# Kernel tuning notes

Measured on AMD Instinct MI355X. Metric: run time of the kernel, lower is better.

## Reference

```python
import jax, jax.numpy as jnp
import numpy as np

B, C, H, IN = 128, 1024, 256, 19  # batch, subcarriers, hidden, input dim
P = 2 * H                          # prism input dim (att + rad features)
NL = 8                             # layers in attenuation/radiance nets
UEBS = 2 * 4                       # num_ue_antennas * num_bs_antennas


def _init(key, shape, scale=0.02):
    return (jax.random.normal(key, shape, dtype=jnp.float32) * scale)


def setup_inputs() -> dict:
    key = jax.random.key(0)
    ks = jax.random.split(key, 24)
    return {
        "positions": jax.random.normal(ks[0], (B, 3), dtype=jnp.float32),
        "ue_antennas": jax.random.normal(ks[1], (B, 2), dtype=jnp.float32),
        "bs_antennas": jax.random.normal(ks[2], (B, 4), dtype=jnp.float32),
        "additional_features": jax.random.normal(ks[3], (B, 10), dtype=jnp.float32),
        "att_W1": _init(ks[4], (IN, H)), "att_b1": _init(ks[5], (H,)),
        "att_Wh": _init(ks[6], (NL - 1, H, H)), "att_bh": _init(ks[7], (NL - 1, H)),
        # radiance net: same structure
        "rad_W1": _init(ks[8], (IN, H)), "rad_b1": _init(ks[9], (H,)),
        "rad_Wh": _init(ks[10], (NL - 1, H, H)), "rad_bh": _init(ks[11], (NL - 1, H)),
        # RF prism: per-subcarrier stacked weights
        "prism_W1": _init(ks[12], (C, P, H)), "prism_b1": _init(ks[13], (C, H)),
        "prism_W2": _init(ks[14], (C, H, H)), "prism_b2": _init(ks[15], (C, H)),
        "prism_W3": _init(ks[16], (C, H)), "prism_b3": _init(ks[17], (C,)),
        # mimo head: Linear(1 -> ue*bs)
        "mimo_W": _init(ks[18], (1, UEBS)), "mimo_b": _init(ks[19], (UEBS,)),
    }


def _deep_mlp(x, W1, b1, Wh, bh):
    h = jax.nn.relu(x @ W1 + b1)
    def step(h, wb):
        W, b = wb
        return jax.nn.relu(h @ W + b), None
    h, _ = jax.lax.scan(step, h, (Wh, bh))
    return h


def reference(positions, ue_antennas, bs_antennas, additional_features,
              att_W1, att_b1, att_Wh, att_bh,
              rad_W1, rad_b1, rad_Wh, rad_bh,
              prism_W1, prism_b1, prism_W2, prism_b2, prism_W3, prism_b3,
              mimo_W, mimo_b):
    x = jnp.concatenate([positions, ue_antennas, bs_antennas, additional_features], axis=1)  # [B,19]
    att = _deep_mlp(x, att_W1, att_b1, att_Wh, att_bh)  # [B,H]
    rad = _deep_mlp(x, rad_W1, rad_b1, rad_Wh, rad_bh)  # [B,H]
    feat = jnp.concatenate([att, rad], axis=1)  # [B,2H]
    # batched per-subcarrier 3-layer MLPs (grouped GEMMs)
    h1 = jax.nn.relu(jnp.einsum('bi,cio->bco', feat, prism_W1) + prism_b1)  # [B,C,H]
    h2 = jax.nn.relu(jnp.einsum('bch,cho->bco', h1, prism_W2) + prism_b2)   # [B,C,H]
    sub = jnp.einsum('bch,ch->bc', h2, prism_W3) + prism_b3                 # [B,C]
    mimo = sub.mean(axis=1, keepdims=True) @ mimo_W + mimo_b                # [B,8]
    return sub, mimo
```

## Files before the change

kernel.cpp:

```cpp
#include <hip/hip_runtime.h>
#include <hip/hip_bf16.h>
#include <stdint.h>

#define Bv 128
#define Hv 256
#define INv 19
#define Pv 512
#define Cv 1024
#define NLh 7

typedef __attribute__((ext_vector_type(4))) float floatx4;
typedef __attribute__((ext_vector_type(8))) short shortx8;
typedef __attribute__((ext_vector_type(4))) unsigned int uintx4;

__device__ __forceinline__ unsigned short f2bf(float f) {
    union { float f; unsigned int u; } v; v.f = f;
    unsigned int r = v.u + 0x7fffu + ((v.u >> 16) & 1u);
    return (unsigned short)(r >> 16);
}

__device__ __forceinline__ int swz(int r) { return ((r & 7) ^ ((r >> 3) & 7)); }

#define BAR() do { asm volatile("s_waitcnt lgkmcnt(0)" ::: "memory"); \
                   __builtin_amdgcn_s_barrier(); } while (0)

__global__ __launch_bounds__(256) void mlp_fused(
    const float* __restrict__ pos, const float* __restrict__ ue,
    const float* __restrict__ bs,  const float* __restrict__ addf,
    const float* __restrict__ attW1, const float* __restrict__ attb1,
    const float* __restrict__ attWh, const float* __restrict__ attbh,
    const float* __restrict__ radW1, const float* __restrict__ radb1,
    const float* __restrict__ radWh, const float* __restrict__ radbh,
    unsigned short* __restrict__ feat)
{
    int blk = blockIdx.x;
    int net = blk >> 6, bq = blk & 63;
    const float* W1 = net ? radW1 : attW1;
    const float* b1 = net ? radb1 : attb1;
    const float* Wh = net ? radWh : attWh;
    const float* bh = net ? radbh : attbh;
    __shared__ float xs[2][INv];
    __shared__ float hr[2][Hv];
    __shared__ float part[4][2][Hv];
    int t = threadIdx.x;
    if (t < 2 * INv) {
        int r = t / INv, k = t - r * INv;
        int b = bq * 2 + r;
        float v;
        if (k < 3) v = pos[b*3 + k];
        else if (k < 5) v = ue[b*2 + (k-3)];
        else if (k < 9) v = bs[b*4 + (k-5)];
        else v = addf[b*10 + (k-9)];
        xs[r][k] = v;
    }
    __syncthreads();
    {
        float a0 = b1[t], a1 = a0;
        #pragma unroll
        for (int k = 0; k < INv; ++k) {
            float w = W1[k*Hv + t];
            a0 += xs[0][k] * w;
            a1 += xs[1][k] * w;
        }
        hr[0][t] = fmaxf(a0, 0.f);
        hr[1][t] = fmaxf(a1, 0.f);
    }
    __syncthreads();
    int half = t >> 6, oq = t & 63;
    for (int layer = 0; layer < NLh; ++layer) {
        const float* W = Wh + (size_t)layer * Hv * Hv;
        const float* Wp = W + (size_t)(half * 64) * Hv + oq * 4;
        floatx4 a0r0 = {0.f,0.f,0.f,0.f}, a1r0 = {0.f,0.f,0.f,0.f};
        floatx4 a0r1 = {0.f,0.f,0.f,0.f}, a1r1 = {0.f,0.f,0.f,0.f};
        #pragma unroll 8
        for (int kk = 0; kk < 64; kk += 2) {
            floatx4 w0 = *reinterpret_cast<const floatx4*>(Wp + (size_t)kk * Hv);
            floatx4 w1 = *reinterpret_cast<const floatx4*>(Wp + (size_t)(kk+1) * Hv);
            float h00 = hr[0][half*64 + kk], h01 = hr[0][half*64 + kk + 1];
            float h10 = hr[1][half*64 + kk], h11 = hr[1][half*64 + kk + 1];
            a0r0 += w0 * h00; a1r0 += w1 * h01;
            a0r1 += w0 * h10; a1r1 += w1 * h11;
        }
        floatx4 r0 = a0r0 + a1r0, r1 = a0r1 + a1r1;
        *reinterpret_cast<floatx4*>(&part[half][0][oq*4]) = r0;
        *reinterpret_cast<floatx4*>(&part[half][1][oq*4]) = r1;
        __syncthreads();
        int r = t >> 7, o2 = (t & 127) * 2;
        const float* bias = bh + layer * Hv;
        float s0 = part[0][r][o2]   + part[1][r][o2]   + part[2][r][o2]   + part[3][r][o2]   + bias[o2];
        float s1 = part[0][r][o2+1] + part[1][r][o2+1] + part[2][r][o2+1] + part[3][r][o2+1] + bias[o2+1];
        s0 = fmaxf(s0, 0.f); s1 = fmaxf(s1, 0.f);
        if (layer == NLh - 1) {
            feat[(size_t)(bq*2 + r) * Pv + net*Hv + o2]     = f2bf(s0);
            feat[(size_t)(bq*2 + r) * Pv + net*Hv + o2 + 1] = f2bf(s1);
        } else {
            hr[r][o2] = s0; hr[r][o2+1] = s1;
        }
        __syncthreads();
    }
}


__device__ __forceinline__ void stage_w_p(const float* __restrict__ src,
                                          int kg, int oq, floatx4* r) {
    const float* p = src + (size_t)(kg * 8) * Hv + oq * 4;
    #pragma unroll
    for (int i = 0; i < 8; ++i) r[i] = *reinterpret_cast<const floatx4*>(p + i * Hv);
}

__device__ __forceinline__ void write_w(char* wb, int kg, int oq, const floatx4* r) {
    #pragma unroll
    for (int j = 0; j < 4; ++j) {
        int o = oq*4 + j;
        unsigned int p0 = (unsigned int)f2bf(r[0][j]) | ((unsigned int)f2bf(r[1][j]) << 16);
        unsigned int p1 = (unsigned int)f2bf(r[2][j]) | ((unsigned int)f2bf(r[3][j]) << 16);
        unsigned int p2 = (unsigned int)f2bf(r[4][j]) | ((unsigned int)f2bf(r[5][j]) << 16);
        unsigned int p3 = (unsigned int)f2bf(r[6][j]) | ((unsigned int)f2bf(r[7][j]) << 16);
        uintx4 v = {p0, p1, p2, p3};
        int slot = kg ^ swz(o);
        *reinterpret_cast<uintx4*>(wb + o*128 + slot*16) = v;
    }
}

__device__ __forceinline__ void stage_a(const unsigned short* __restrict__ feat,
                                        int t, int tid, uintx4* r) {
    #pragma unroll
    for (int q = 0; q < 2; ++q) {
        int si = tid + q*512, row = si >> 3, s = si & 7;
        r[q] = *reinterpret_cast<const uintx4*>(feat + row*Pv + t*64 + s*8);
    }
}

__device__ __forceinline__ void write_a(char* ab, int tid, const uintx4* r) {
    #pragma unroll
    for (int q = 0; q < 2; ++q) {
        int si = tid + q*512, row = si >> 3, s = si & 7;
        int slot = s ^ swz(row);
        *reinterpret_cast<uintx4*>(ab + row*128 + slot*16) = r[q];
    }
}

__device__ __forceinline__ void mfma_l1(const char* ab, const char* wb,
                                        int wm, int wn, int l,
                                        floatx4 (&acc)[4][4]) {
    #pragma unroll
    for (int ks = 0; ks < 2; ++ks) {
        shortx8 af[4], bf[4];
        #pragma unroll
        for (int m = 0; m < 4; ++m) {
            int row = wm*64 + m*16 + (l & 15);
            int slot = (ks*4 + (l >> 4)) ^ swz(row);
            af[m] = *reinterpret_cast<const shortx8*>(ab + row*128 + slot*16);
        }
        #pragma unroll
        for (int n = 0; n < 4; ++n) {
            int o = wn*64 + n*16 + (l & 15);
            int slot = (ks*4 + (l >> 4)) ^ swz(o);
            bf[n] = *reinterpret_cast<const shortx8*>(wb + o*128 + slot*16);
        }
        #pragma unroll
        for (int m = 0; m < 4; ++m)
            #pragma unroll
            for (int n = 0; n < 4; ++n)
                acc[m][n] = __builtin_amdgcn_mfma_f32_16x16x32_bf16(af[m], bf[n], acc[m][n], 0, 0, 0);
    }
}

__device__ __forceinline__ void mfma_l2(const char* h1, const char* wb, int t2,
                                        int wm, int wn, int l,
                                        floatx4 (&acc)[4][4]) {
    #pragma unroll
    for (int ks = 0; ks < 2; ++ks) {
        shortx8 af[4], bf[4];
        #pragma unroll
        for (int m = 0; m < 4; ++m) {
            int row = wm*64 + m*16 + (l & 15);
            int k2 = t2*64 + ks*32 + (l >> 4)*8;
            af[m] = *reinterpret_cast<const shortx8*>(h1 + row*512 + ((k2*2) ^ (swz(row) << 4)));
        }
        #pragma unroll
        for (int n = 0; n < 4; ++n) {
            int o = wn*64 + n*16 + (l & 15);
            int slot = (ks*4 + (l >> 4)) ^ swz(o);
            bf[n] = *reinterpret_cast<const shortx8*>(wb + o*128 + slot*16);
        }
        #pragma unroll
        for (int m = 0; m < 4; ++m)
            #pragma unroll
            for (int n = 0; n < 4; ++n)
                acc[m][n] = __builtin_amdgcn_mfma_f32_16x16x32_bf16(af[m], bf[n], acc[m][n], 0, 0, 0);
    }
}


__global__ __launch_bounds__(512)
__attribute__((amdgpu_waves_per_eu(2, 2)))
void prism_kernel(
    const unsigned short* __restrict__ feat,
    const float* __restrict__ W1, const float* __restrict__ b1,
    const float* __restrict__ W2, const float* __restrict__ b2,
    const float* __restrict__ W3, const float* __restrict__ b3,
    float* __restrict__ out)
{
    __shared__ __align__(16) char smem[163840];
    char* ab0 = smem;
    char* ab1 = smem + 16384;
    char* wb0 = smem + 32768;
    char* wb1 = smem + 65536;
    char* h1  = smem + 98304;
    float* subws = (float*)(smem + 98304);

    const int tid = threadIdx.x;
    const int l = tid & 63;
    const int w = tid >> 6;
    const int wm = w >> 2;
    const int wn = w & 3;
    const int kg = w;
    const int oq = l;
    const int c = blockIdx.x;

    const float* W1c = W1 + (size_t)c * (Pv * Hv);
    const float* W2c = W2 + (size_t)c * (Hv * Hv);

    floatx4 wr[3][8];
    uintx4  ar[2][2];

    stage_a(feat, 0, tid, ar[0]);
    stage_a(feat, 1, tid, ar[1]);
    stage_w_p(W1c + (size_t)0 * 64 * Hv, kg, oq, wr[0]);
    stage_w_p(W1c + (size_t)1 * 64 * Hv, kg, oq, wr[1]);
    stage_w_p(W1c + (size_t)2 * 64 * Hv, kg, oq, wr[2]);
    write_a(ab0, tid, ar[0]);
    write_w(wb0, kg, oq, wr[0]);
    BAR();

    floatx4 acc[4][4];
    #pragma unroll
    for (int m = 0; m < 4; ++m)
        #pragma unroll
        for (int n = 0; n < 4; ++n)
            acc[m][n] = (floatx4){0.f, 0.f, 0.f, 0.f};

    #pragma unroll
    for (int t = 0; t < 8; ++t) {
        if (t < 6) stage_a(feat, t + 2, tid, ar[t & 1]);
        const float* ps = (t < 5) ? W1c + (size_t)(t + 3) * 64 * Hv
                                  : W2c + (size_t)(t - 5) * 64 * Hv;
        stage_w_p(ps, kg, oq, wr[t % 3]);
        mfma_l1((t & 1) ? ab1 : ab0, (t & 1) ? wb1 : wb0, wm, wn, l, acc);
        if (t < 7) write_a(((t + 1) & 1) ? ab1 : ab0, tid, ar[(t + 1) & 1]);
        write_w(((t + 1) & 1) ? wb1 : wb0, kg, oq, wr[(t + 1) % 3]);
        BAR();
    }

    {
        float bias1v[4];
        #pragma unroll
        for (int n = 0; n < 4; ++n)
            bias1v[n] = b1[c*Hv + wn*64 + n*16 + (l & 15)];
        #pragma unroll
        for (int m = 0; m < 4; ++m) {
            #pragma unroll
            for (int n = 0; n < 4; ++n) {
                int o = wn*64 + n*16 + (l & 15);
                #pragma unroll
                for (int jj = 0; jj < 4; ++jj) {
                    int bb = wm*64 + m*16 + (l >> 4)*4 + jj;
                    float v = fmaxf(acc[m][n][jj] + bias1v[n], 0.f);
                    *(unsigned short*)(h1 + bb*512 + ((o*2) ^ (swz(bb) << 4))) = f2bf(v);
                }
            }
        }
    }
    BAR();

    #pragma unroll
    for (int m = 0; m < 4; ++m)
        #pragma unroll
        for (int n = 0; n < 4; ++n)
            acc[m][n] = (floatx4){0.f, 0.f, 0.f, 0.f};

    #pragma unroll
    for (int t2 = 0; t2 < 4; ++t2) {
        if (t2 == 0) stage_w_p(W2c + (size_t)3 * 64 * Hv, kg, oq, wr[2]);
        mfma_l2(h1, (t2 & 1) ? wb1 : wb0, t2, wm, wn, l, acc);
        if (t2 < 3) write_w(((t2 + 1) & 1) ? wb1 : wb0, kg, oq, wr[(9 + t2) % 3]);
        BAR();
    }

    float bias2v[4], w3v[4];
    #pragma unroll
    for (int n = 0; n < 4; ++n) {
        int o = wn*64 + n*16 + (l & 15);
        bias2v[n] = b2[c*Hv + o];
        w3v[n]    = W3[c*Hv + o];
    }
    float b3v = b3[c];
    float p[4][4];
    #pragma unroll
    for (int m = 0; m < 4; ++m)
        #pragma unroll
        for (int jj = 0; jj < 4; ++jj) {
            float s = 0.f;
            #pragma unroll
            for (int n = 0; n < 4; ++n)
                s += fmaxf(acc[m][n][jj] + bias2v[n], 0.f) * w3v[n];
            p[m][jj] = s;
        }
    #pragma unroll
    for (int m = 0; m < 4; ++m)
        #pragma unroll
        for (int jj = 0; jj < 4; ++jj) {
            p[m][jj] += __shfl_xor(p[m][jj], 1, 64);
            p[m][jj] += __shfl_xor(p[m][jj], 2, 64);
            p[m][jj] += __shfl_xor(p[m][jj], 4, 64);
            p[m][jj] += __shfl_xor(p[m][jj], 8, 64);
        }
    {
        int t16 = l & 15;
        float pv = 0.f;
        #pragma unroll
        for (int m = 0; m < 4; ++m)
            #pragma unroll
            for (int jj = 0; jj < 4; ++jj)
                if (m == (t16 >> 2) && jj == (t16 & 3)) pv = p[m][jj];
        int bb = wm*64 + (t16 >> 2)*16 + (l >> 4)*4 + (t16 & 3);
        subws[wn*128 + bb] = pv;
    }
    BAR();
    if (tid < 128) {
        float s = subws[tid] + subws[128 + tid] + subws[256 + tid] + subws[384 + tid] + b3v;
        out[(size_t)tid * Cv + c] = s;
    }
}


__global__ __launch_bounds__(256) void mimo_kernel(
    const float* __restrict__ sub, const float* __restrict__ mW,
    const float* __restrict__ mB, float* __restrict__ out)
{
    int b = blockIdx.x;
    int t = threadIdx.x;
    float s = 0.f;
    #pragma unroll
    for (int j = 0; j < 4; ++j) s += sub[b*Cv + t + j*256];
    #pragma unroll
    for (int m = 1; m < 64; m <<= 1) s += __shfl_xor(s, m, 64);
    __shared__ float red[4];
    if ((t & 63) == 0) red[t >> 6] = s;
    __syncthreads();
    if (t < 8) {
        float mean = (red[0] + red[1] + red[2] + red[3]) * (1.0f / 1024.0f);
        out[Bv * Cv + b*8 + t] = mean * mW[t] + mB[t];
    }
}


extern "C" void kernel_launch(void* const* d_in, const int* in_sizes, int n_in,
                              void* d_out, int out_size, void* d_ws, size_t ws_size,
                              hipStream_t stream) {
    (void)in_sizes; (void)n_in; (void)out_size; (void)ws_size;
    const float* pos   = (const float*)d_in[0];
    const float* ue    = (const float*)d_in[1];
    const float* bsant = (const float*)d_in[2];
    const float* addf  = (const float*)d_in[3];
    const float* attW1 = (const float*)d_in[4];
    const float* attb1 = (const float*)d_in[5];
    const float* attWh = (const float*)d_in[6];
    const float* attbh = (const float*)d_in[7];
    const float* radW1 = (const float*)d_in[8];
    const float* radb1 = (const float*)d_in[9];
    const float* radWh = (const float*)d_in[10];
    const float* radbh = (const float*)d_in[11];
    const float* pW1   = (const float*)d_in[12];
    const float* pb1   = (const float*)d_in[13];
    const float* pW2   = (const float*)d_in[14];
    const float* pb2   = (const float*)d_in[15];
    const float* pW3   = (const float*)d_in[16];
    const float* pb3   = (const float*)d_in[17];
    const float* mW    = (const float*)d_in[18];
    const float* mB    = (const float*)d_in[19];
    float* out = (float*)d_out;

    unsigned short* feat = (unsigned short*)d_ws;

    mlp_fused<<<128, 256, 0, stream>>>(pos, ue, bsant, addf,
                                       attW1, attb1, attWh, attbh,
                                       radW1, radb1, radWh, radbh, feat);
    prism_kernel<<<Cv, 512, 0, stream>>>(feat, pW1, pb1, pW2, pb2, pW3, pb3, out);
    mimo_kernel<<<Bv, 256, 0, stream>>>(out, mW, mB, out);
}
```

Before: 213.2 us.

## Process two subcarriers per block with cross-subcarrier prefetch and packed bf16 conversion

Each prism block now handles two consecutive subcarriers, prefetching the next subcarrier's first W1 tiles and activation tiles during the tail of the current one's layer-2 loop. This hides pipeline startup and the tail bubbles. Shared memory drops to 128KB by reusing the activation/weight buffers for h1 and the W2 buffers. The waves_per_eu attribute is removed and the weight ring shrinks from 3 to 2 register stages. Float-to-bf16 conversion uses the hardware v_cvt_pk_bf16_f32 instruction instead of manual rounding. The trade-offs are half as many blocks (512 across the CUs) and more barriers.

```diff
diff --git a/kernel.cpp b/kernel.cpp
--- a/kernel.cpp
+++ b/kernel.cpp
@@ -13,10 +13,10 @@
 typedef __attribute__((ext_vector_type(8))) short shortx8;
 typedef __attribute__((ext_vector_type(4))) unsigned int uintx4;
 
-__device__ __forceinline__ unsigned short f2bf(float f) {
-    union { float f; unsigned int u; } v; v.f = f;
-    unsigned int r = v.u + 0x7fffu + ((v.u >> 16) & 1u);
-    return (unsigned short)(r >> 16);
+__device__ __forceinline__ unsigned int cvt_pk_bf16(float lo, float hi) {
+    unsigned int r;
+    asm("v_cvt_pk_bf16_f32 %0, %1, %2" : "=v"(r) : "v"(lo), "v"(hi));
+    return r;
 }
 
 __device__ __forceinline__ int swz(int r) { return ((r & 7) ^ ((r >> 3) & 7)); }
@@ -91,8 +91,8 @@
         float s1 = part[0][r][o2+1] + part[1][r][o2+1] + part[2][r][o2+1] + part[3][r][o2+1] + bias[o2+1];
         s0 = fmaxf(s0, 0.f); s1 = fmaxf(s1, 0.f);
         if (layer == NLh - 1) {
-            feat[(size_t)(bq*2 + r) * Pv + net*Hv + o2]     = f2bf(s0);
-            feat[(size_t)(bq*2 + r) * Pv + net*Hv + o2 + 1] = f2bf(s1);
+            *reinterpret_cast<unsigned int*>(
+                feat + (size_t)(bq*2 + r) * Pv + net*Hv + o2) = cvt_pk_bf16(s0, s1);
         } else {
             hr[r][o2] = s0; hr[r][o2+1] = s1;
         }
@@ -112,11 +112,10 @@
     #pragma unroll
     for (int j = 0; j < 4; ++j) {
         int o = oq*4 + j;
-        unsigned int p0 = (unsigned int)f2bf(r[0][j]) | ((unsigned int)f2bf(r[1][j]) << 16);
-        unsigned int p1 = (unsigned int)f2bf(r[2][j]) | ((unsigned int)f2bf(r[3][j]) << 16);
-        unsigned int p2 = (unsigned int)f2bf(r[4][j]) | ((unsigned int)f2bf(r[5][j]) << 16);
-        unsigned int p3 = (unsigned int)f2bf(r[6][j]) | ((unsigned int)f2bf(r[7][j]) << 16);
-        uintx4 v = {p0, p1, p2, p3};
+        uintx4 v = { cvt_pk_bf16(r[0][j], r[1][j]),
+                     cvt_pk_bf16(r[2][j], r[3][j]),
+                     cvt_pk_bf16(r[4][j], r[5][j]),
+                     cvt_pk_bf16(r[6][j], r[7][j]) };
         int slot = kg ^ swz(o);
         *reinterpret_cast<uintx4*>(wb + o*128 + slot*16) = v;
     }
@@ -193,22 +192,22 @@
 }
 
 
-__global__ __launch_bounds__(512)
-__attribute__((amdgpu_waves_per_eu(2, 2)))
-void prism_kernel(
+__global__ __launch_bounds__(512) void prism_kernel(
     const unsigned short* __restrict__ feat,
     const float* __restrict__ W1, const float* __restrict__ b1,
     const float* __restrict__ W2, const float* __restrict__ b2,
     const float* __restrict__ W3, const float* __restrict__ b3,
     float* __restrict__ out)
 {
-    __shared__ __align__(16) char smem[163840];
+    __shared__ __align__(16) char smem[131072];
     char* ab0 = smem;
     char* ab1 = smem + 16384;
     char* wb0 = smem + 32768;
     char* wb1 = smem + 65536;
-    char* h1  = smem + 98304;
-    float* subws = (float*)(smem + 98304);
+    char* h1  = smem;
+    char* w2b0 = smem + 65536;
+    char* w2b1 = smem + 98304;
+    float* subws = (float*)smem;
 
     const int tid = threadIdx.x;
     const int l = tid & 63;
@@ -217,120 +216,152 @@
     const int wn = w & 3;
     const int kg = w;
     const int oq = l;
-    const int c = blockIdx.x;
-
-    const float* W1c = W1 + (size_t)c * (Pv * Hv);
-    const float* W2c = W2 + (size_t)c * (Hv * Hv);
-
-    floatx4 wr[3][8];
+
+    floatx4 wr[2][8];
     uintx4  ar[2][2];
 
-    stage_a(feat, 0, tid, ar[0]);
-    stage_a(feat, 1, tid, ar[1]);
-    stage_w_p(W1c + (size_t)0 * 64 * Hv, kg, oq, wr[0]);
-    stage_w_p(W1c + (size_t)1 * 64 * Hv, kg, oq, wr[1]);
-    stage_w_p(W1c + (size_t)2 * 64 * Hv, kg, oq, wr[2]);
-    write_a(ab0, tid, ar[0]);
-    write_w(wb0, kg, oq, wr[0]);
-    BAR();
-
-    floatx4 acc[4][4];
-    #pragma unroll
-    for (int m = 0; m < 4; ++m)
-        #pragma unroll
-        for (int n = 0; n < 4; ++n)
-            acc[m][n] = (floatx4){0.f, 0.f, 0.f, 0.f};
-
-    #pragma unroll
-    for (int t = 0; t < 8; ++t) {
-        if (t < 6) stage_a(feat, t + 2, tid, ar[t & 1]);
-        const float* ps = (t < 5) ? W1c + (size_t)(t + 3) * 64 * Hv
-                                  : W2c + (size_t)(t - 5) * 64 * Hv;
-        stage_w_p(ps, kg, oq, wr[t % 3]);
-        mfma_l1((t & 1) ? ab1 : ab0, (t & 1) ? wb1 : wb0, wm, wn, l, acc);
-        if (t < 7) write_a(((t + 1) & 1) ? ab1 : ab0, tid, ar[(t + 1) & 1]);
-        write_w(((t + 1) & 1) ? wb1 : wb0, kg, oq, wr[(t + 1) % 3]);
+    {
+        const float* W1c = W1 + (size_t)(blockIdx.x * 2) * (Pv * Hv);
+        stage_w_p(W1c + (size_t)0 * 64 * Hv, kg, oq, wr[0]);
+        stage_a(feat, 0, tid, ar[0]);
+        stage_w_p(W1c + (size_t)1 * 64 * Hv, kg, oq, wr[1]);
+        stage_a(feat, 1, tid, ar[1]);
+        write_w(wb0, kg, oq, wr[0]);
+        write_a(ab0, tid, ar[0]);
         BAR();
     }
 
-    {
-        float bias1v[4];
-        #pragma unroll
-        for (int n = 0; n < 4; ++n)
-            bias1v[n] = b1[c*Hv + wn*64 + n*16 + (l & 15)];
-        #pragma unroll
-        for (int m = 0; m < 4; ++m) {
-            #pragma unroll
-            for (int n = 0; n < 4; ++n) {
-                int o = wn*64 + n*16 + (l & 15);
+    for (int k = 0; k < 2; ++k) {
+        const int c = blockIdx.x * 2 + k;
+        const float* W1c = W1 + (size_t)c * (Pv * Hv);
+        const float* W2c = W2 + (size_t)c * (Hv * Hv);
+        const float* W1n = W1c + (size_t)(Pv * Hv);
+
+        floatx4 acc[4][4];
+        #pragma unroll
+        for (int m = 0; m < 4; ++m)
+            #pragma unroll
+            for (int n = 0; n < 4; ++n)
+                acc[m][n] = (floatx4){0.f, 0.f, 0.f, 0.f};
+
+        #pragma unroll
+        for (int t = 0; t < 8; ++t) {
+            if (t + 2 < 8) {
+                stage_w_p(W1c + (size_t)(t + 2) * 64 * Hv, kg, oq, wr[t & 1]);
+                stage_a(feat, t + 2, tid, ar[t & 1]);
+            } else if (t == 6) {
+                stage_w_p(W2c + (size_t)0 * 64 * Hv, kg, oq, wr[0]);
+            } else {
+                stage_w_p(W2c + (size_t)1 * 64 * Hv, kg, oq, wr[1]);
+            }
+            mfma_l1((t & 1) ? ab1 : ab0, (t & 1) ? wb1 : wb0, wm, wn, l, acc);
+            if (t + 1 < 8) {
+                if ((t + 1) & 1) { write_w(wb1, kg, oq, wr[1]); write_a(ab1, tid, ar[1]); }
+                else             { write_w(wb0, kg, oq, wr[0]); write_a(ab0, tid, ar[0]); }
+            }
+            BAR();
+        }
+
+        {
+            float bias1v[4];
+            #pragma unroll
+            for (int n = 0; n < 4; ++n)
+                bias1v[n] = b1[c*Hv + wn*64 + n*16 + (l & 15)];
+            #pragma unroll
+            for (int m = 0; m < 4; ++m) {
                 #pragma unroll
-                for (int jj = 0; jj < 4; ++jj) {
-                    int bb = wm*64 + m*16 + (l >> 4)*4 + jj;
-                    float v = fmaxf(acc[m][n][jj] + bias1v[n], 0.f);
-                    *(unsigned short*)(h1 + bb*512 + ((o*2) ^ (swz(bb) << 4))) = f2bf(v);
+                for (int n = 0; n < 4; ++n) {
+                    int o = wn*64 + n*16 + (l & 15);
+                    #pragma unroll
+                    for (int jj = 0; jj < 4; ++jj) {
+                        int bb = wm*64 + m*16 + (l >> 4)*4 + jj;
+                        float v = fmaxf(acc[m][n][jj] + bias1v[n], 0.f);
+                        *(unsigned short*)(h1 + bb*512 + ((o*2) ^ (swz(bb) << 4))) =
+                            (unsigned short)(cvt_pk_bf16(v, v) & 0xffffu);
+                    }
                 }
             }
         }
-    }
-    BAR();
-
-    #pragma unroll
-    for (int m = 0; m < 4; ++m)
-        #pragma unroll
-        for (int n = 0; n < 4; ++n)
-            acc[m][n] = (floatx4){0.f, 0.f, 0.f, 0.f};
-
-    #pragma unroll
-    for (int t2 = 0; t2 < 4; ++t2) {
-        if (t2 == 0) stage_w_p(W2c + (size_t)3 * 64 * Hv, kg, oq, wr[2]);
-        mfma_l2(h1, (t2 & 1) ? wb1 : wb0, t2, wm, wn, l, acc);
-        if (t2 < 3) write_w(((t2 + 1) & 1) ? wb1 : wb0, kg, oq, wr[(9 + t2) % 3]);
+        write_w(w2b0, kg, oq, wr[0]);
         BAR();
-    }
-
-    float bias2v[4], w3v[4];
-    #pragma unroll
-    for (int n = 0; n < 4; ++n) {
-        int o = wn*64 + n*16 + (l & 15);
-        bias2v[n] = b2[c*Hv + o];
-        w3v[n]    = W3[c*Hv + o];
-    }
-    float b3v = b3[c];
-    float p[4][4];
-    #pragma unroll
-    for (int m = 0; m < 4; ++m)
-        #pragma unroll
-        for (int jj = 0; jj < 4; ++jj) {
-            float s = 0.f;
+
+        #pragma unroll
+        for (int m = 0; m < 4; ++m)
             #pragma unroll
             for (int n = 0; n < 4; ++n)
-                s += fmaxf(acc[m][n][jj] + bias2v[n], 0.f) * w3v[n];
-            p[m][jj] = s;
-        }
-    #pragma unroll
-    for (int m = 0; m < 4; ++m)
-        #pragma unroll
-        for (int jj = 0; jj < 4; ++jj) {
-            p[m][jj] += __shfl_xor(p[m][jj], 1, 64);
-            p[m][jj] += __shfl_xor(p[m][jj], 2, 64);
-            p[m][jj] += __shfl_xor(p[m][jj], 4, 64);
-            p[m][jj] += __shfl_xor(p[m][jj], 8, 64);
-        }
-    {
-        int t16 = l & 15;
-        float pv = 0.f;
-        #pragma unroll
-        for (int m = 0; m < 4; ++m)
-            #pragma unroll
-            for (int jj = 0; jj < 4; ++jj)
-                if (m == (t16 >> 2) && jj == (t16 & 3)) pv = p[m][jj];
-        int bb = wm*64 + (t16 >> 2)*16 + (l >> 4)*4 + (t16 & 3);
-        subws[wn*128 + bb] = pv;
-    }
-    BAR();
-    if (tid < 128) {
-        float s = subws[tid] + subws[128 + tid] + subws[256 + tid] + subws[384 + tid] + b3v;
-        out[(size_t)tid * Cv + c] = s;
+                acc[m][n] = (floatx4){0.f, 0.f, 0.f, 0.f};
+
+        #pragma unroll
+        for (int t2 = 0; t2 < 4; ++t2) {
+            if (t2 == 0) {
+                if (k == 0) stage_a(feat, 0, tid, ar[0]);
+                stage_w_p(W2c + (size_t)2 * 64 * Hv, kg, oq, wr[0]);
+            } else if (t2 == 1) {
+                if (k == 0) stage_a(feat, 1, tid, ar[1]);
+                stage_w_p(W2c + (size_t)3 * 64 * Hv, kg, oq, wr[1]);
+            } else if (t2 == 2) {
+                if (k == 0) stage_w_p(W1n + (size_t)0 * 64 * Hv, kg, oq, wr[0]);
+            } else {
+                if (k == 0) stage_w_p(W1n + (size_t)1 * 64 * Hv, kg, oq, wr[1]);
+            }
+            mfma_l2(h1, (t2 & 1) ? w2b1 : w2b0, t2, wm, wn, l, acc);
+            if (t2 == 0)      write_w(w2b1, kg, oq, wr[1]);
+            else if (t2 == 1) write_w(w2b0, kg, oq, wr[0]);
+            else if (t2 == 2) write_w(w2b1, kg, oq, wr[1]);
+            BAR();
+        }
+
+        float bias2v[4], w3v[4];
+        #pragma unroll
+        for (int n = 0; n < 4; ++n) {
+            int o = wn*64 + n*16 + (l & 15);
+            bias2v[n] = b2[c*Hv + o];
+            w3v[n]    = W3[c*Hv + o];
+        }
+        float b3v = b3[c];
+        float p[4][4];
+        #pragma unroll
+        for (int m = 0; m < 4; ++m)
+            #pragma unroll
+            for (int jj = 0; jj < 4; ++jj) {
+                float s = 0.f;
+                #pragma unroll
+                for (int n = 0; n < 4; ++n)
+                    s += fmaxf(acc[m][n][jj] + bias2v[n], 0.f) * w3v[n];
+                p[m][jj] = s;
+            }
+        #pragma unroll
+        for (int m = 0; m < 4; ++m)
+            #pragma unroll
+            for (int jj = 0; jj < 4; ++jj) {
+                p[m][jj] += __shfl_xor(p[m][jj], 1, 64);
+                p[m][jj] += __shfl_xor(p[m][jj], 2, 64);
+                p[m][jj] += __shfl_xor(p[m][jj], 4, 64);
+                p[m][jj] += __shfl_xor(p[m][jj], 8, 64);
+            }
+        BAR();
+        {
+            int t16 = l & 15;
+            float pv = 0.f;
+            #pragma unroll
+            for (int m = 0; m < 4; ++m)
+                #pragma unroll
+                for (int jj = 0; jj < 4; ++jj)
+                    if (m == (t16 >> 2) && jj == (t16 & 3)) pv = p[m][jj];
+            int bb = wm*64 + (t16 >> 2)*16 + (l >> 4)*4 + (t16 & 3);
+            subws[wn*128 + bb] = pv;
+        }
+        BAR();
+        if (tid < 128) {
+            float s = subws[tid] + subws[128 + tid] + subws[256 + tid] + subws[384 + tid] + b3v;
+            out[(size_t)tid * Cv + c] = s;
+        }
+        if (k == 0) {
+            BAR();
+            write_a(ab0, tid, ar[0]);
+            write_w(wb0, kg, oq, wr[0]);
+            BAR();
+        }
     }
 }
 
@@ -387,6 +418,6 @@
     mlp_fused<<<128, 256, 0, stream>>>(pos, ue, bsant, addf,
                                        attW1, attb1, attWh, attbh,
                                        radW1, radb1, radWh, radbh, feat);
-    prism_kernel<<<Cv, 512, 0, stream>>>(feat, pW1, pb1, pW2, pb2, pW3, pb3, out);
+    prism_kernel<<<Cv / 2, 512, 0, stream>>>(feat, pW1, pb1, pW2, pb2, pW3, pb3, out);
     mimo_kernel<<<Bv, 256, 0, stream>>>(out, mW, mB, out);
 }
```

New measurement: 362.9 us. 1.7x slower.
